# Performance work log

Measured on AMD Instinct MI355X. Metric: run time of the kernel, lower is better.

## Reference

```python
import jax, jax.numpy as jnp
import numpy as np

B, N, M, D = 4, 16384, 4096, 64


def setup_inputs() -> dict:
    key = jax.random.key(0)
    k1, k2, k3 = jax.random.split(key, 3)
    pointcloud = jax.random.normal(k1, (B, N, 3), dtype=jnp.float32)
    keys = jax.random.normal(k2, (M, 3), dtype=jnp.float32)
    values = jax.random.normal(k3, (M, D), dtype=jnp.float32)
    return {"pointcloud": pointcloud, "keys": keys, "values": values}


def reference(pointcloud, keys, values):
    # Nearest-key quantization: argmin over squared L2 distances.
    # Expand ||p - k||^2 = ||p||^2 - 2 p.k + ||k||^2 (GEMM form; avoids the
    # (B,N,M,3) broadcasted diff tensor of the original).
    p_sq = jnp.sum(pointcloud * pointcloud, axis=-1, keepdims=True)      # (B,N,1)
    k_sq = jnp.sum(keys * keys, axis=-1)                                  # (M,)
    cross = jnp.einsum('bnc,mc->bnm', pointcloud, keys)                   # (B,N,M)
    d2 = p_sq - 2.0 * cross + k_sq[None, None, :]                         # (B,N,M)
    ids = jnp.argmin(d2, axis=-1)                                         # (B,N) int
    # Embedding lookup (get_features): gather rows of the value table.
    feats = values[ids]                                                   # (B,N,D)
    return feats, ids[..., None], pointcloud
```

## Files before the change

kernel.cpp:

```cpp
#include <hip/hip_runtime.h>

#pragma clang fp contract(off)

#define BB 4
#define NN 16384
#define MM 4096
#define DD 64
#define BN (BB * NN)
#define FEATS_OFF 0
#define IDS_OFF (BN * DD)
#define PC_OFF (IDS_OFF + BN)

#define CC 8
#define PP 4
#define PPB (256 * PP / CC)
#define KPL (MM / CC)

__global__ __launch_bounds__(256, 2)
void quant_embed_kernel(const float* __restrict__ pc,
                        const float* __restrict__ keys,
                        const float* __restrict__ values,
                        float* __restrict__ out)
{
#pragma clang fp contract(off)
    __shared__ float4 skeys[MM];

    const int tid = threadIdx.x;

    #pragma unroll
    for (int i = 0; i < MM / 256; ++i) {
        const int m = tid + i * 256;
        const float kx = keys[3 * m + 0];
        const float ky = keys[3 * m + 1];
        const float kz = keys[3 * m + 2];
        const float ksq = ((kx * kx) + (ky * ky)) + (kz * kz);
        skeys[m] = make_float4(2.0f * kx, 2.0f * ky, 2.0f * kz, ksq);
    }

    {
        const int base = blockIdx.x * (PPB * 3 / 4);
        if (tid < PPB * 3 / 4) {
            ((float4*)(out + PC_OFF))[base + tid] =
                ((const float4*)pc)[base + tid];
        }
    }

    const int chunk = tid & (CC - 1);
    const int g = tid >> 3;
    const int p0 = blockIdx.x * PPB + g * PP;

    float px[PP], py[PP], pz[PP], psq[PP], bd[PP];
    int bk[PP];
    #pragma unroll
    for (int i = 0; i < PP; ++i) {
        px[i] = pc[3 * (p0 + i) + 0];
        py[i] = pc[3 * (p0 + i) + 1];
        pz[i] = pc[3 * (p0 + i) + 2];
        psq[i] = ((px[i] * px[i]) + (py[i] * py[i])) + (pz[i] * pz[i]);
        bd[i] = 3.402823466e38f;
        bk[i] = 0;
    }

    __syncthreads();

    #pragma unroll 4
    for (int k = 0; k < KPL; ++k) {
        const float4 K = skeys[(k << 3) + chunk];
        #pragma unroll
        for (int i = 0; i < PP; ++i) {
            const float cross2 = ((px[i] * K.x) + (py[i] * K.y)) + (pz[i] * K.z);
            const float d2 = (psq[i] - cross2) + K.w;
            const bool lt = d2 < bd[i];
            bd[i] = lt ? d2 : bd[i];
            bk[i] = lt ? k  : bk[i];
        }
    }

    int bid[PP];
    #pragma unroll
    for (int i = 0; i < PP; ++i) {
        float d = bd[i];
        int   m = (bk[i] << 3) + chunk;
        #pragma unroll
        for (int off = 1; off <= 4; off <<= 1) {
            const float od = __shfl_xor(d, off);
            const int   om = __shfl_xor(m, off);
            if (od < d || (od == d && om < m)) { d = od; m = om; }
        }
        bid[i] = m;
    }

    #pragma unroll
    for (int i = 0; i < PP; ++i) {
        const float4* vrow = (const float4*)(values + (size_t)bid[i] * DD);
        float4* of4 = (float4*)(out + FEATS_OFF + (size_t)(p0 + i) * DD);
        of4[chunk * 2 + 0] = vrow[chunk * 2 + 0];
        of4[chunk * 2 + 1] = vrow[chunk * 2 + 1];
        if (chunk == 0) out[IDS_OFF + p0 + i] = (float)bid[i];
    }
}

extern "C" void kernel_launch(void* const* d_in, const int* in_sizes, int n_in,
                              void* d_out, int out_size, void* d_ws, size_t ws_size,
                              hipStream_t stream) {
    const float* pc     = (const float*)d_in[0];
    const float* keys   = (const float*)d_in[1];
    const float* values = (const float*)d_in[2];
    float* out = (float*)d_out;

    dim3 grid(BN / PPB);
    dim3 block(256);
    quant_embed_kernel<<<grid, block, 0, stream>>>(pc, keys, values, out);
}
```

Measured before the change: 127.4 us.

## Raise points per thread and pack key pairs into split shared arrays

Each thread now handles 8 points against key pairs stored as two float4 arrays, so each shared-memory read serves two keys and more points. The reduction widens to 16 lanes, and point coordinates and gather/store use vectorized float4 loads. The aim is to raise the ratio of arithmetic to LDS traffic in the argmin loop. It costs more registers per thread, with a possible occupancy loss, and tracks absolute key indices in the inner loop.

```diff
diff --git a/kernel.cpp b/kernel.cpp
--- a/kernel.cpp
+++ b/kernel.cpp
@@ -2,19 +2,18 @@
 
 #pragma clang fp contract(off)
 
-#define BB 4
-#define NN 16384
 #define MM 4096
 #define DD 64
-#define BN (BB * NN)
+#define BN 65536
 #define FEATS_OFF 0
 #define IDS_OFF (BN * DD)
 #define PC_OFF (IDS_OFF + BN)
 
-#define CC 8
-#define PP 4
-#define PPB (256 * PP / CC)
-#define KPL (MM / CC)
+#define CC 16
+#define PP 8
+#define PPB 128
+#define NPAIR (MM / 2)
+#define KIT (MM / (2 * CC))
 
 __global__ __launch_bounds__(256, 2)
 void quant_embed_kernel(const float* __restrict__ pc,
@@ -23,18 +22,21 @@
                         float* __restrict__ out)
 {
 #pragma clang fp contract(off)
-    __shared__ float4 skeys[MM];
+    __shared__ float4 skA[NPAIR];
+    __shared__ float4 skB[NPAIR];
 
     const int tid = threadIdx.x;
 
     #pragma unroll
-    for (int i = 0; i < MM / 256; ++i) {
-        const int m = tid + i * 256;
-        const float kx = keys[3 * m + 0];
-        const float ky = keys[3 * m + 1];
-        const float kz = keys[3 * m + 2];
-        const float ksq = ((kx * kx) + (ky * ky)) + (kz * kz);
-        skeys[m] = make_float4(2.0f * kx, 2.0f * ky, 2.0f * kz, ksq);
+    for (int i = 0; i < NPAIR / 256; ++i) {
+        const int j = tid + i * 256;
+        const float2 f0 = ((const float2*)keys)[3 * j + 0];
+        const float2 f1 = ((const float2*)keys)[3 * j + 1];
+        const float2 f2 = ((const float2*)keys)[3 * j + 2];
+        const float ksq0 = ((f0.x * f0.x) + (f0.y * f0.y)) + (f1.x * f1.x);
+        const float ksq1 = ((f1.y * f1.y) + (f2.x * f2.x)) + (f2.y * f2.y);
+        skA[j] = make_float4(2.0f * f0.x, 2.0f * f1.y, 2.0f * f0.y, 2.0f * f2.x);
+        skB[j] = make_float4(2.0f * f1.x, 2.0f * f2.y, ksq0, ksq1);
     }
 
     {
@@ -45,58 +47,70 @@
         }
     }
 
-    const int chunk = tid & (CC - 1);
-    const int g = tid >> 3;
+    const int c = tid & (CC - 1);
+    const int g = tid >> 4;
     const int p0 = blockIdx.x * PPB + g * PP;
 
+    float arr[24];
+    {
+        const float4* pcv = (const float4*)(pc + 3 * p0);
+        #pragma unroll
+        for (int i = 0; i < 6; ++i) ((float4*)arr)[i] = pcv[i];
+    }
     float px[PP], py[PP], pz[PP], psq[PP], bd[PP];
-    int bk[PP];
+    int bm[PP];
     #pragma unroll
     for (int i = 0; i < PP; ++i) {
-        px[i] = pc[3 * (p0 + i) + 0];
-        py[i] = pc[3 * (p0 + i) + 1];
-        pz[i] = pc[3 * (p0 + i) + 2];
+        px[i] = arr[3 * i + 0];
+        py[i] = arr[3 * i + 1];
+        pz[i] = arr[3 * i + 2];
         psq[i] = ((px[i] * px[i]) + (py[i] * py[i])) + (pz[i] * pz[i]);
         bd[i] = 3.402823466e38f;
-        bk[i] = 0;
+        bm[i] = 0;
     }
 
     __syncthreads();
 
-    #pragma unroll 4
-    for (int k = 0; k < KPL; ++k) {
-        const float4 K = skeys[(k << 3) + chunk];
+    #pragma unroll 2
+    for (int k = 0; k < KIT; ++k) {
+        const int j = (k << 4) + c;
+        const float4 A  = skA[j];
+        const float4 Bv = skB[j];
+        const int m0 = (k << 5) + (c << 1);
+        const int m1 = m0 + 1;
         #pragma unroll
         for (int i = 0; i < PP; ++i) {
-            const float cross2 = ((px[i] * K.x) + (py[i] * K.y)) + (pz[i] * K.z);
-            const float d2 = (psq[i] - cross2) + K.w;
-            const bool lt = d2 < bd[i];
-            bd[i] = lt ? d2 : bd[i];
-            bk[i] = lt ? k  : bk[i];
+            const float ca = ((px[i] * A.x) + (py[i] * A.z)) + (pz[i] * Bv.x);
+            const float da = (psq[i] - ca) + Bv.z;
+            const bool lta = da < bd[i];
+            bd[i] = lta ? da : bd[i];
+            bm[i] = lta ? m0 : bm[i];
+            const float cb = ((px[i] * A.y) + (py[i] * A.w)) + (pz[i] * Bv.y);
+            const float db = (psq[i] - cb) + Bv.w;
+            const bool ltb = db < bd[i];
+            bd[i] = ltb ? db : bd[i];
+            bm[i] = ltb ? m1 : bm[i];
         }
     }
 
-    int bid[PP];
     #pragma unroll
     for (int i = 0; i < PP; ++i) {
         float d = bd[i];
-        int   m = (bk[i] << 3) + chunk;
+        int   m = bm[i];
         #pragma unroll
-        for (int off = 1; off <= 4; off <<= 1) {
+        for (int off = 1; off < CC; off <<= 1) {
             const float od = __shfl_xor(d, off);
             const int   om = __shfl_xor(m, off);
             if (od < d || (od == d && om < m)) { d = od; m = om; }
         }
-        bid[i] = m;
+        bm[i] = m;
     }
 
     #pragma unroll
     for (int i = 0; i < PP; ++i) {
-        const float4* vrow = (const float4*)(values + (size_t)bid[i] * DD);
-        float4* of4 = (float4*)(out + FEATS_OFF + (size_t)(p0 + i) * DD);
-        of4[chunk * 2 + 0] = vrow[chunk * 2 + 0];
-        of4[chunk * 2 + 1] = vrow[chunk * 2 + 1];
-        if (chunk == 0) out[IDS_OFF + p0 + i] = (float)bid[i];
+        const float4* vrow = (const float4*)(values + (size_t)bm[i] * DD);
+        ((float4*)(out + FEATS_OFF + (size_t)(p0 + i) * DD))[c] = vrow[c];
+        if (c == 0) out[IDS_OFF + p0 + i] = (float)bm[i];
     }
 }
 
```

Result: no change. 125.8 us (-1.3%).
